# Performance work log

Hardware: AMD Instinct MI355X
Metric: run time of the kernel (lower is better)

## Reference

```python
import jax, jax.numpy as jnp
import numpy as np

B, S, HID = 2, 2048, 1024
H, D = 16, 64
R = 128  # max_relative_position
NREL = 2 * R + 1


def _make_indices():
    i = np.arange(S)[:, None]
    j = np.arange(S)[None, :]
    return np.clip(j - i + R, 0, 2 * R).astype(np.int32)  # [S, S]


def setup_inputs() -> dict:
    key = jax.random.key(0)
    ks = jax.random.split(key, 10)
    sc = 0.02
    return {
        "hidden_states": jax.random.normal(ks[0], (B, S, HID), jnp.float32),
        "st_mask": jnp.ones((B, S), jnp.float32),
        "Wq": jax.random.normal(ks[1], (HID, HID), jnp.float32) * sc,
        "bq": jnp.zeros((HID,), jnp.float32),
        "Wk": jax.random.normal(ks[2], (HID, HID), jnp.float32) * sc,
        "bk": jnp.zeros((HID,), jnp.float32),
        "Wv": jax.random.normal(ks[3], (HID, HID), jnp.float32) * sc,
        "bv": jnp.zeros((HID,), jnp.float32),
        "rel_key_emb": jax.random.normal(ks[4], (NREL, D), jnp.float32) * sc,
        "rel_val_emb": jax.random.normal(ks[5], (NREL, D), jnp.float32) * sc,
        "indices": jnp.asarray(_make_indices()),
    }


def reference(hidden_states, st_mask, Wq, bq, Wk, bk, Wv, bv, rel_key_emb, rel_val_emb, indices):
    b, s, _ = hidden_states.shape

    def heads(x):  # [B,S,HID] -> [B,H,S,D]
        return x.reshape(b, s, H, D).transpose(0, 2, 1, 3)

    q = heads(hidden_states @ Wq.T + bq)
    k = heads(hidden_states @ Wk.T + bk)
    v = heads(hidden_states @ Wv.T + bv)

    scores = jnp.einsum("bhqd,bhkd->bhqk", q, k) / jnp.sqrt(jnp.asarray(D, q.dtype))

    # relative position key bias: gather per (query, key) pair
    rel_scores = jnp.einsum("bhqd,rd->bhqr", q, rel_key_emb)  # [B,H,S,NREL]
    idx = indices[None, None]  # [1,1,S,S]
    scores = scores + jnp.take_along_axis(rel_scores, jnp.broadcast_to(idx, scores.shape), axis=3)

    mask = (1.0 - st_mask) * -10000.0  # [B,S]
    scores = scores + mask[:, None, None, :]

    probs = jax.nn.softmax(scores, axis=-1)  # dropout is identity at eval
    context = jnp.einsum("bhqk,bhkd->bhqd", probs, v)

    # scatter-add probs back onto relative buckets for the value path
    qi = jnp.arange(s)[:, None]  # [S,1] broadcasts with indices [S,S]
    rel_probs = jnp.zeros((b, H, s, NREL), probs.dtype).at[:, :, qi, indices].add(probs)
    context = context + jnp.einsum("bhqr,rd->bhqd", rel_probs, rel_val_emb)

    return context.transpose(0, 2, 1, 3).reshape(b, s, H * D)
```

## Files before the change

kernel.cpp:

```cpp
#include <hip/hip_runtime.h>
#include <math.h>

typedef __bf16 bf16;
typedef __bf16 bf16x8 __attribute__((ext_vector_type(8)));
typedef __bf16 bf16x4 __attribute__((ext_vector_type(4)));
typedef float  f32x4  __attribute__((ext_vector_type(4)));

namespace {
constexpr int B_ = 2, S_ = 2048, HID_ = 1024, H_ = 16, D_ = 64, R_ = 128, NREL_ = 257;
constexpr float LOG2E_ = 1.44269504f;
constexpr float QSC_ = 0.125f * LOG2E_;
}

static __device__ __forceinline__ f32x4 mfma16(bf16x8 a, bf16x8 b, f32x4 c) {
  return __builtin_amdgcn_mfma_f32_16x16x32_bf16(a, b, c, 0, 0, 0);
}
static __device__ __forceinline__ void split2(float f, bf16 &hi, bf16 &lo) {
  hi = (bf16)f; lo = (bf16)(f - (float)hi);
}
static __device__ __forceinline__ void gload16(const bf16* g, bf16* l) {
  __builtin_amdgcn_global_load_lds(
      (const __attribute__((address_space(1))) void*)g,
      (__attribute__((address_space(3))) void*)l, 16, 0, 0);
}

__global__ __launch_bounds__(256) void prep_kernel(
    const float* __restrict__ st_mask, const float* __restrict__ rkE,
    const float* __restrict__ rvE, const float* __restrict__ hidden,
    const float* __restrict__ Wq, const float* __restrict__ Wk,
    const float* __restrict__ Wv,
    float* __restrict__ msk2, bf16* __restrict__ rkEb, bf16* __restrict__ rvTb,
    bf16* __restrict__ Ahg, bf16* __restrict__ Alg, bf16* __restrict__ Wbg)
{
  const int t0 = blockIdx.x * 256 + threadIdx.x;
  const int NT = gridDim.x * 256;
  for (int t = t0; t < B_ * S_; t += NT)
    msk2[t] = (1.f - st_mask[t]) * -10000.f * LOG2E_;
  for (int t = t0; t < 272 * 64; t += NT) {
    const int bk = t >> 6, d = t & 63;
    rkEb[t] = (bk < NREL_) ? (bf16)(rkE[bk * D_ + d] * 8.0f) : (bf16)0.f;
  }
  for (int t = t0; t < 64 * 288; t += NT) {
    const int d = t / 288, c = t - d * 288;
    rvTb[t] = (c < NREL_) ? (bf16)rvE[c * D_ + d] : (bf16)0.f;
  }
  for (int t = t0; t < (B_ * S_ * HID_) / 4; t += NT) {
    const float4 a = ((const float4*)hidden)[t];
    const float av[4] = {a.x, a.y, a.z, a.w};
    bf16x4 h, o;
#pragma unroll
    for (int i = 0; i < 4; ++i) {
      bf16 th, tl;
      split2(av[i], th, tl);
      h[i] = th; o[i] = tl;
    }
    *(bf16x4*)&Ahg[t * 4] = h;
    *(bf16x4*)&Alg[t * 4] = o;
  }
  for (int t = t0; t < 3 * (HID_ * HID_) / 4; t += NT) {
    const int s = t >> 18, i = t & 262143;
    const float4 wv4 = ((const float4*)(s == 0 ? Wq : s == 1 ? Wk : Wv))[i];
    bf16x4 h;
    h[0] = (bf16)wv4.x; h[1] = (bf16)wv4.y; h[2] = (bf16)wv4.z; h[3] = (bf16)wv4.w;
    *(bf16x4*)&Wbg[s * 1048576 + i * 4] = h;
  }
}

__global__ __launch_bounds__(256, 2) void qkv_mfma_kernel(
    const bf16* __restrict__ Ahg, const bf16* __restrict__ Alg,
    const bf16* __restrict__ Wbg,
    const float* __restrict__ bq, const float* __restrict__ bk,
    const float* __restrict__ bv,
    bf16* __restrict__ Qh, bf16* __restrict__ Ql,
    bf16* __restrict__ Kb, bf16* __restrict__ Vt)
{
  const int swz = ((int)blockIdx.x & 7) * 64 + ((int)blockIdx.x >> 3);
  const int m0 = (swz >> 4) * 128;
  const int n0 = (swz & 15) * 64;
  const int tid = threadIdx.x;
  const int l = tid & 63, w = tid >> 6;
  const int cl = l & 15, g = l >> 4;

  __shared__ __align__(16) bf16 AhS[2][4096];
  __shared__ __align__(16) bf16 AlS[2][4096];
  __shared__ __align__(16) bf16 WS[2][3][2048];

  const int r0 = tid >> 2;
  const int csw = (((tid & 3) ^ (r0 & 3)) << 3);
  const size_t aoff0 = (size_t)(m0 + r0) * HID_ + csw;
  const size_t aoff1 = (size_t)(m0 + 64 + r0) * HID_ + csw;
  const size_t woff  = (size_t)(n0 + r0) * HID_ + csw;
  const int wb = w * 512;

  const int rA0 = w * 16 + cl;
  const int eA0 = rA0 * 32 + 8 * (g ^ (rA0 & 3));
  const int eA1 = eA0 + 2048;
  const int eW  = cl * 32 + 8 * (g ^ (cl & 3));

  f32x4 acc[2][3][4];
#pragma unroll
  for (int hf = 0; hf < 2; ++hf)
#pragma unroll
    for (int s = 0; s < 3; ++s)
#pragma unroll
      for (int nf = 0; nf < 4; ++nf)
#pragma unroll
        for (int i = 0; i < 4; ++i) acc[hf][s][nf][i] = 0.f;

  gload16(Ahg + aoff0, &AhS[0][wb]);
  gload16(Ahg + aoff1, &AhS[0][2048 + wb]);
  gload16(Alg + aoff0, &AlS[0][wb]);
  gload16(Alg + aoff1, &AlS[0][2048 + wb]);
  gload16(Wbg + woff,           &WS[0][0][wb]);
  gload16(Wbg + 1048576 + woff, &WS[0][1][wb]);
  gload16(Wbg + 2097152 + woff, &WS[0][2][wb]);
  __syncthreads();

  int cur = 0;
  for (int kt = 0; kt < HID_ / 32; ++kt) {
    if (kt + 1 < HID_ / 32) {
      const size_t ko = (size_t)(kt + 1) * 32;
      bf16* ah = &AhS[cur ^ 1][0]; bf16* al = &AlS[cur ^ 1][0];
      gload16(Ahg + aoff0 + ko, ah + wb);
      gload16(Ahg + aoff1 + ko, ah + 2048 + wb);
      gload16(Alg + aoff0 + ko, al + wb);
      gload16(Alg + aoff1 + ko, al + 2048 + wb);
      gload16(Wbg + woff + ko,           &WS[cur ^ 1][0][wb]);
      gload16(Wbg + 1048576 + woff + ko, &WS[cur ^ 1][1][wb]);
      gload16(Wbg + 2097152 + woff + ko, &WS[cur ^ 1][2][wb]);
    }

    const bf16x8 fah0 = *(const bf16x8*)&AhS[cur][eA0];
    const bf16x8 fah1 = *(const bf16x8*)&AhS[cur][eA1];
    const bf16x8 fal0 = *(const bf16x8*)&AlS[cur][eA0];
    const bf16x8 fal1 = *(const bf16x8*)&AlS[cur][eA1];
#pragma unroll
    for (int s = 0; s < 3; ++s)
#pragma unroll
      for (int nf = 0; nf < 4; ++nf) {
        const bf16x8 fb = *(const bf16x8*)&WS[cur][s][nf * 512 + eW];
        acc[0][s][nf] = mfma16(fah0, fb, acc[0][s][nf]);
        acc[0][s][nf] = mfma16(fal0, fb, acc[0][s][nf]);
        acc[1][s][nf] = mfma16(fah1, fb, acc[1][s][nf]);
        acc[1][s][nf] = mfma16(fal1, fb, acc[1][s][nf]);
      }
    __syncthreads();
    cur ^= 1;
  }

  const float* bs_[3] = {bq, bk, bv};
#pragma unroll
  for (int s = 0; s < 3; ++s)
#pragma unroll
    for (int nf = 0; nf < 4; ++nf) {
      const int n = n0 + nf * 16 + cl;
      const float bias = bs_[s][n];
      const int hd = n >> 6, d = n & 63;
#pragma unroll
      for (int hf = 0; hf < 2; ++hf)
#pragma unroll
        for (int reg = 0; reg < 4; ++reg) {
          const int m = m0 + hf * 64 + w * 16 + g * 4 + reg;
          const int b = m >> 11, sq = m & (S_ - 1);
          const float val = acc[hf][s][nf][reg] + bias;
          if (s == 0) {
            bf16 h, o; split2(val * QSC_, h, o);
            const size_t idx = ((size_t)(b * H_ + hd) * S_ + sq) * D_ + d;
            Qh[idx] = h; Ql[idx] = o;
          } else if (s == 1) {
            Kb[((size_t)(b * H_ + hd) * S_ + sq) * D_ + d] = (bf16)val;
          } else {
            Vt[(((size_t)(b * H_ + hd) * (S_ / 64) + (sq >> 6)) * D_ + d) * 64 + (sq & 63)]
                = (bf16)val;
          }
        }
    }
}

__global__ __launch_bounds__(512, 4) void attn_kernel(
    const bf16* __restrict__ Qh, const bf16* __restrict__ Ql,
    const bf16* __restrict__ Kb, const bf16* __restrict__ Vt,
    const float* __restrict__ msk2, const bf16* __restrict__ rkEb,
    const bf16* __restrict__ rvTb, float* __restrict__ out)
{
  const int swz = ((int)blockIdx.x & 7) * 128 + ((int)blockIdx.x >> 3);
  const int qt = swz & 31, h = (swz >> 5) & 15, b = swz >> 9;
  const int q0 = qt * 64;
  const int tid = threadIdx.x;
  const int l = tid & 63, w = tid >> 6;
  const int wq = (w & 3) * 16;
  const int wh = w >> 2;
  const int cl = l & 15, g = l >> 4, kg8 = g * 8;
  const int lq = wq + cl;

  __shared__ __align__(16) bf16 k_s[2][4096];
  __shared__ __align__(16) bf16 v_s[2][4096];
  __shared__ __align__(16) bf16 T[64][288];
  __shared__ __align__(16) bf16 ph[64][72];
  __shared__ float red[2][3][64];
  __shared__ float lsum_s[64];

  const size_t bh = (size_t)(b * H_ + h) * S_;
  const bf16* Kbase = Kb + bh * D_;
  const bf16* Vbase = Vt + bh * D_;
  const float* mbase = msk2 + b * S_;

  const int tKr = tid >> 3;
  const int koff = tKr * 64 + (((tid & 7) ^ (tKr & 7)) << 3);
  const int voff = koff;
  bf16* kdst0 = &k_s[0][w * 512]; bf16* kdst1 = &k_s[1][w * 512];
  bf16* vdst0 = &v_s[0][w * 512]; bf16* vdst1 = &v_s[1][w * 512];

  gload16(Kbase + koff, kdst0);
  gload16(Vbase + voff, vdst0);

  bf16x8 qh0, qh1, ql0, ql1;
  {
    const size_t base = (bh + q0 + lq) * D_ + kg8;
    qh0 = *(const bf16x8*)(Qh + base);
    qh1 = *(const bf16x8*)(Qh + base + 32);
    ql0 = *(const bf16x8*)(Ql + base);
    ql1 = *(const bf16x8*)(Ql + base + 32);
  }

  {
    const int nt0 = wh ? 9 : 0, ntE = wh ? 17 : 9;
    for (int nt = nt0; nt < ntE; ++nt) {
      f32x4 r; r[0] = r[1] = r[2] = r[3] = 0.f;
      const bf16x8 a0 = *(const bf16x8*)(rkEb + (size_t)(nt * 16 + cl) * 64 + kg8);
      const bf16x8 a1 = *(const bf16x8*)(rkEb + (size_t)(nt * 16 + cl) * 64 + 32 + kg8);
      r = mfma16(a0, qh0, r); r = mfma16(a0, ql0, r);
      r = mfma16(a1, qh1, r); r = mfma16(a1, ql1, r);
      bf16x4 pk;
#pragma unroll
      for (int reg = 0; reg < 4; ++reg) pk[reg] = (bf16)r[reg];
      *(bf16x4*)&T[lq][nt * 16 + g * 4] = pk;
    }
  }
  __syncthreads();

  const float rs_lo = (float)T[lq][0];
  const float rs_hi = (float)T[lq][2 * R_];
  const int qg = q0 + lq;

  f32x4 ctx0, ctx1;
#pragma unroll
  for (int i = 0; i < 4; ++i) { ctx0[i] = 0.f; ctx1[i] = 0.f; }
  float lsum = 0.f, plo = 0.f, phi = 0.f;

  const int r00 = wh * 32 + cl, r10 = wh * 32 + 16 + cl;
  const int e00 = r00 * 64 + 8 * (g ^ (r00 & 7)), e01 = r00 * 64 + 8 * ((4 + g) ^ (r00 & 7));
  const int e10 = r10 * 64 + 8 * (g ^ (r10 & 7)), e11 = r10 * 64 + 8 * ((4 + g) ^ (r10 & 7));
  const int f0  = e00, f0b = e01;
  const int f1  = e10, f1b = e11;

  int cur = 0;
  for (int kt = 0; kt < S_ / 64; ++kt) {
    if (kt + 1 < S_ / 64) {
      gload16(Kbase + (size_t)(kt + 1) * 4096 + koff, cur ? kdst0 : kdst1);
      gload16(Vbase + (size_t)(kt + 1) * 4096 + voff, cur ? vdst0 : vdst1);
    }

    const bf16* kc = &k_s[cur][0];
    const bf16x8 a00 = *(const bf16x8*)&kc[e00];
    const bf16x8 a01 = *(const bf16x8*)&kc[e01];
    const bf16x8 a10 = *(const bf16x8*)&kc[e10];
    const bf16x8 a11 = *(const bf16x8*)&kc[e11];

    f32x4 s0, s1;
    s0[0]=s0[1]=s0[2]=s0[3]=0.f; s1[0]=s1[1]=s1[2]=s1[3]=0.f;
    __builtin_amdgcn_s_setprio(1);
    s0 = mfma16(a00, qh0, s0); s0 = mfma16(a00, ql0, s0);
    s0 = mfma16(a01, qh1, s0); s0 = mfma16(a01, ql1, s0);
    s1 = mfma16(a10, qh0, s1); s1 = mfma16(a10, ql0, s1);
    s1 = mfma16(a11, qh1, s1); s1 = mfma16(a11, ql1, s1);
    __builtin_amdgcn_s_setprio(0);

    const int j0 = kt * 64 + wh * 32;
    const float4 mk0 = *(const float4*)(mbase + j0 + g * 4);
    const float4 mk1 = *(const float4*)(mbase + j0 + 16 + g * 4);
    const int dlt = kt * 64 - q0;
    const int mode = (dlt <= -192) ? 0 : (dlt >= 192 ? 1 : 2);

#pragma unroll
    for (int nf = 0; nf < 2; ++nf) {
      const f32x4 sa = nf ? s1 : s0;
      const float4 mkv = nf ? mk1 : mk0;
      const float mks[4] = {mkv.x, mkv.y, mkv.z, mkv.w};
      float p[4];
      if (mode == 0) {
#pragma unroll
        for (int reg = 0; reg < 4; ++reg) p[reg] = exp2f(sa[reg] + rs_lo + mks[reg]);
        plo += (p[0] + p[1]) + (p[2] + p[3]);
      } else if (mode == 1) {
#pragma unroll
        for (int reg = 0; reg < 4; ++reg) p[reg] = exp2f(sa[reg] + rs_hi + mks[reg]);
        phi += (p[0] + p[1]) + (p[2] + p[3]);
      } else {
        const int jb = j0 + nf * 16 + g * 4;
#pragma unroll
        for (int reg = 0; reg < 4; ++reg) {
          const int bkv = jb + reg - qg + R_;
          const int bkc = bkv < 0 ? 0 : (bkv > 2 * R_ ? 2 * R_ : bkv);
          const float pv = exp2f(sa[reg] + (float)T[lq][bkc] + mks[reg]);
          p[reg] = pv;
          if (bkv <= 0)           plo += pv;
          else if (bkv >= 2 * R_) phi += pv;
          else                    T[lq][bkv] = (bf16)pv;
        }
      }
      lsum += (p[0] + p[1]) + (p[2] + p[3]);
      bf16x4 pk;
#pragma unroll
      for (int reg = 0; reg < 4; ++reg) pk[reg] = (bf16)p[reg];
      *(bf16x4*)&ph[lq][wh * 32 + nf * 16 + g * 4] = pk;
    }
    __syncthreads();

    const bf16x8 pa0 = *(const bf16x8*)&ph[lq][kg8];
    const bf16x8 pa1 = *(const bf16x8*)&ph[lq][32 + kg8];
    const bf16* vc = &v_s[cur][0];
    const bf16x8 vb00 = *(const bf16x8*)&vc[f0];
    const bf16x8 vb01 = *(const bf16x8*)&vc[f0b];
    const bf16x8 vb10 = *(const bf16x8*)&vc[f1];
    const bf16x8 vb11 = *(const bf16x8*)&vc[f1b];
    __builtin_amdgcn_s_setprio(1);
    ctx0 = mfma16(pa0, vb00, ctx0); ctx0 = mfma16(pa1, vb01, ctx0);
    ctx1 = mfma16(pa0, vb10, ctx1); ctx1 = mfma16(pa1, vb11, ctx1);
    __builtin_amdgcn_s_setprio(0);
    __syncthreads();
    cur ^= 1;
  }

  lsum += __shfl_xor(lsum, 16); lsum += __shfl_xor(lsum, 32);
  plo  += __shfl_xor(plo, 16);  plo  += __shfl_xor(plo, 32);
  phi  += __shfl_xor(phi, 16);  phi  += __shfl_xor(phi, 32);
  if (l < 16) {
    red[wh][0][wq + l] = lsum;
    red[wh][1][wq + l] = plo;
    red[wh][2][wq + l] = phi;
  }
  __syncthreads();
  if (tid < 64) {
    lsum_s[tid]    = red[0][0][tid] + red[1][0][tid];
    T[tid][0]      = (bf16)(red[0][1][tid] + red[1][1][tid]);
    T[tid][2 * R_] = (bf16)(red[0][2][tid] + red[1][2][tid]);
  }
  for (int t = tid; t < 64 * 32; t += 512) {
    const int c = t & 31;
    if (c) T[t >> 5][256 + c] = (bf16)0.f;
  }
  if (q0 < R_ || q0 > S_ - R_ - 64) {
    for (int t = tid; t < 64 * 256; t += 512) {
      const int r = t >> 8, c = t & 255;
      if (c >= 1) {
        const int j = q0 + r + c - R_;
        if (j < 0 || j >= S_) T[r][c] = (bf16)0.f;
      }
    }
  }
  __syncthreads();

#pragma unroll
  for (int ks = 0; ks < 9; ++ks) {
    const bf16x8 pa = *(const bf16x8*)&T[lq][ks * 32 + kg8];
    const bf16x8 v0 = *(const bf16x8*)(rvTb + (size_t)(wh * 32 + cl) * 288 + ks * 32 + kg8);
    const bf16x8 v1 = *(const bf16x8*)(rvTb + (size_t)(wh * 32 + 16 + cl) * 288 + ks * 32 + kg8);
    __builtin_amdgcn_s_setprio(1);
    ctx0 = mfma16(pa, v0, ctx0);
    ctx1 = mfma16(pa, v1, ctx1);
    __builtin_amdgcn_s_setprio(0);
  }

#pragma unroll
  for (int reg = 0; reg < 4; ++reg) {
    const int qrow = wq + g * 4 + reg;
    const float invl = 1.f / lsum_s[qrow];
    float* op = out + (size_t)(b * S_ + q0 + qrow) * HID_ + h * 64 + wh * 32;
    op[cl]      = ctx0[reg] * invl;
    op[16 + cl] = ctx1[reg] * invl;
  }
}

extern "C" void kernel_launch(void* const* d_in, const int* in_sizes, int n_in,
                              void* d_out, int out_size, void* d_ws, size_t ws_size,
                              hipStream_t stream)
{
  (void)in_sizes; (void)n_in; (void)out_size; (void)ws_size;
  const float* hidden  = (const float*)d_in[0];
  const float* st_mask = (const float*)d_in[1];
  const float* Wq = (const float*)d_in[2];
  const float* bq = (const float*)d_in[3];
  const float* Wk = (const float*)d_in[4];
  const float* bk = (const float*)d_in[5];
  const float* Wv = (const float*)d_in[6];
  const float* bv = (const float*)d_in[7];
  const float* rkE = (const float*)d_in[8];
  const float* rvE = (const float*)d_in[9];
  float* out = (float*)d_out;

  const size_t per = (size_t)B_ * H_ * S_ * D_;
  char* wsb = (char*)d_ws;
  float* msk2 = (float*)wsb;
  bf16*  rkEb = (bf16*)(wsb + 16384);
  bf16*  rvTb = (bf16*)(wsb + 16384 + 34816);
  char*  base1 = wsb + 16384 + 34816 + 36864;
  bf16* Qh = (bf16*)base1;
  bf16* Ql = Qh + per;
  bf16* Kb = Ql + per;
  bf16* Vt = Kb + per;
  bf16* Ahg = Vt + per;
  bf16* Alg = Ahg + per;
  bf16* Wbg = Alg + per;

  prep_kernel<<<dim3(1024), 256, 0, stream>>>(
      st_mask, rkE, rvE, hidden, Wq, Wk, Wv, msk2, rkEb, rvTb, Ahg, Alg, Wbg);
  qkv_mfma_kernel<<<dim3(512), 256, 0, stream>>>(
      Ahg, Alg, Wbg, bq, bk, bv, Qh, Ql, Kb, Vt);
  attn_kernel<<<dim3(1024), 512, 0, stream>>>(
      Qh, Ql, Kb, Vt, msk2, rkEb, rvTb, out);
}
```

Baseline: 184.1 us.

## Keep P in registers for PV MFMA, split keys across wave halves, reduce ctx at end

Each wave now feeds its own softmax probabilities straight from registers into the PV MFMA. To make that work, V is stored in a permuted column order that matches the MFMA operand layout, and each wave-half accumulates all 64 output dims over its 32 keys. This removes the LDS round-trip for P and one __syncthreads per key tile. In exchange it doubles the context accumulators per wave and adds a final cross-wave reduction through shared memory, which reuses the K/V buffer space.

Measured after the change: 179.7 us. -2.4%, faster.

```diff
diff --git a/kernel.cpp b/kernel.cpp
--- a/kernel.cpp
+++ b/kernel.cpp
@@ -170,7 +170,10 @@
           } else if (s == 1) {
             Kb[((size_t)(b * H_ + hd) * S_ + sq) * D_ + d] = (bf16)val;
           } else {
-            Vt[(((size_t)(b * H_ + hd) * (S_ / 64) + (sq >> 6)) * D_ + d) * 64 + (sq & 63)]
+            const int jo = sq & 63;
+            const int mc = (jo & 32) | (((jo >> 3) & 1) << 4) | (((jo >> 2) & 1) << 3)
+                         | (((jo >> 4) & 1) << 2) | (jo & 3);
+            Vt[(((size_t)(b * H_ + hd) * (S_ / 64) + (sq >> 6)) * D_ + d) * 64 + mc]
                 = (bf16)val;
           }
         }
@@ -193,12 +196,16 @@
   const int cl = l & 15, g = l >> 4, kg8 = g * 8;
   const int lq = wq + cl;
 
-  __shared__ __align__(16) bf16 k_s[2][4096];
-  __shared__ __align__(16) bf16 v_s[2][4096];
+  __shared__ __align__(16) unsigned char U[36864];
   __shared__ __align__(16) bf16 T[64][288];
-  __shared__ __align__(16) bf16 ph[64][72];
   __shared__ float red[2][3][64];
   __shared__ float lsum_s[64];
+
+  bf16* kb0 = (bf16*)&U[0];
+  bf16* kb1 = (bf16*)&U[8192];
+  bf16* vb0 = (bf16*)&U[16384];
+  bf16* vb1 = (bf16*)&U[24576];
+  float* ctxredf = (float*)&U[0];
 
   const size_t bh = (size_t)(b * H_ + h) * S_;
   const bf16* Kbase = Kb + bh * D_;
@@ -207,12 +214,9 @@
 
   const int tKr = tid >> 3;
   const int koff = tKr * 64 + (((tid & 7) ^ (tKr & 7)) << 3);
-  const int voff = koff;
-  bf16* kdst0 = &k_s[0][w * 512]; bf16* kdst1 = &k_s[1][w * 512];
-  bf16* vdst0 = &v_s[0][w * 512]; bf16* vdst1 = &v_s[1][w * 512];
-
-  gload16(Kbase + koff, kdst0);
-  gload16(Vbase + voff, vdst0);
+
+  gload16(Kbase + koff, kb0 + w * 512);
+  gload16(Vbase + koff, vb0 + w * 512);
 
   bf16x8 qh0, qh1, ql0, ql1;
   {
@@ -243,25 +247,31 @@
   const float rs_hi = (float)T[lq][2 * R_];
   const int qg = q0 + lq;
 
-  f32x4 ctx0, ctx1;
-#pragma unroll
-  for (int i = 0; i < 4; ++i) { ctx0[i] = 0.f; ctx1[i] = 0.f; }
+  f32x4 ctx[4];
+#pragma unroll
+  for (int nf = 0; nf < 4; ++nf) { ctx[nf][0]=0.f; ctx[nf][1]=0.f; ctx[nf][2]=0.f; ctx[nf][3]=0.f; }
   float lsum = 0.f, plo = 0.f, phi = 0.f;
 
   const int r00 = wh * 32 + cl, r10 = wh * 32 + 16 + cl;
   const int e00 = r00 * 64 + 8 * (g ^ (r00 & 7)), e01 = r00 * 64 + 8 * ((4 + g) ^ (r00 & 7));
   const int e10 = r10 * 64 + 8 * (g ^ (r10 & 7)), e11 = r10 * 64 + 8 * ((4 + g) ^ (r10 & 7));
-  const int f0  = e00, f0b = e01;
-  const int f1  = e10, f1b = e11;
+  int fv0, fv1, fv2, fv3;
+  {
+    const int rd0 = 0 * 16 + cl, rd1 = 1 * 16 + cl, rd2 = 2 * 16 + cl, rd3 = 3 * 16 + cl;
+    fv0 = rd0 * 64 + 8 * ((4 * wh + g) ^ (rd0 & 7));
+    fv1 = rd1 * 64 + 8 * ((4 * wh + g) ^ (rd1 & 7));
+    fv2 = rd2 * 64 + 8 * ((4 * wh + g) ^ (rd2 & 7));
+    fv3 = rd3 * 64 + 8 * ((4 * wh + g) ^ (rd3 & 7));
+  }
 
   int cur = 0;
   for (int kt = 0; kt < S_ / 64; ++kt) {
     if (kt + 1 < S_ / 64) {
-      gload16(Kbase + (size_t)(kt + 1) * 4096 + koff, cur ? kdst0 : kdst1);
-      gload16(Vbase + (size_t)(kt + 1) * 4096 + voff, cur ? vdst0 : vdst1);
-    }
-
-    const bf16* kc = &k_s[cur][0];
+      gload16(Kbase + (size_t)(kt + 1) * 4096 + koff, (cur ? kb0 : kb1) + w * 512);
+      gload16(Vbase + (size_t)(kt + 1) * 4096 + koff, (cur ? vb0 : vb1) + w * 512);
+    }
+
+    const bf16* kc = cur ? kb1 : kb0;
     const bf16x8 a00 = *(const bf16x8*)&kc[e00];
     const bf16x8 a01 = *(const bf16x8*)&kc[e01];
     const bf16x8 a10 = *(const bf16x8*)&kc[e10];
@@ -282,6 +292,7 @@
     const int dlt = kt * 64 - q0;
     const int mode = (dlt <= -192) ? 0 : (dlt >= 192 ? 1 : 2);
 
+    bf16x4 pk0, pk1;
 #pragma unroll
     for (int nf = 0; nf < 2; ++nf) {
       const f32x4 sa = nf ? s1 : s0;
@@ -313,20 +324,18 @@
       bf16x4 pk;
 #pragma unroll
       for (int reg = 0; reg < 4; ++reg) pk[reg] = (bf16)p[reg];
-      *(bf16x4*)&ph[lq][wh * 32 + nf * 16 + g * 4] = pk;
-    }
-    __syncthreads();
-
-    const bf16x8 pa0 = *(const bf16x8*)&ph[lq][kg8];
-    const bf16x8 pa1 = *(const bf16x8*)&ph[lq][32 + kg8];
-    const bf16* vc = &v_s[cur][0];
-    const bf16x8 vb00 = *(const bf16x8*)&vc[f0];
-    const bf16x8 vb01 = *(const bf16x8*)&vc[f0b];
-    const bf16x8 vb10 = *(const bf16x8*)&vc[f1];
-    const bf16x8 vb11 = *(const bf16x8*)&vc[f1b];
+      if (nf == 0) pk0 = pk; else pk1 = pk;
+    }
+
+    bf16x8 pa;
+    pa[0] = pk0[0]; pa[1] = pk0[1]; pa[2] = pk0[2]; pa[3] = pk0[3];
+    pa[4] = pk1[0]; pa[5] = pk1[1]; pa[6] = pk1[2]; pa[7] = pk1[3];
+    const bf16* vc = cur ? vb1 : vb0;
     __builtin_amdgcn_s_setprio(1);
-    ctx0 = mfma16(pa0, vb00, ctx0); ctx0 = mfma16(pa1, vb01, ctx0);
-    ctx1 = mfma16(pa0, vb10, ctx1); ctx1 = mfma16(pa1, vb11, ctx1);
+    ctx[0] = mfma16(pa, *(const bf16x8*)&vc[fv0], ctx[0]);
+    ctx[1] = mfma16(pa, *(const bf16x8*)&vc[fv1], ctx[1]);
+    ctx[2] = mfma16(pa, *(const bf16x8*)&vc[fv2], ctx[2]);
+    ctx[3] = mfma16(pa, *(const bf16x8*)&vc[fv3], ctx[3]);
     __builtin_amdgcn_s_setprio(0);
     __syncthreads();
     cur ^= 1;
@@ -341,6 +350,15 @@
     red[wh][2][wq + l] = phi;
   }
   __syncthreads();
+
+  {
+    const int nfs = wh ? 0 : 2;
+#pragma unroll
+    for (int k2 = 0; k2 < 2; ++k2)
+#pragma unroll
+      for (int reg = 0; reg < 4; ++reg)
+        ctxredf[((wh * 64) + wq + g * 4 + reg) * 36 + k2 * 16 + cl] = ctx[nfs + k2][reg];
+  }
   if (tid < 64) {
     lsum_s[tid]    = red[0][0][tid] + red[1][0][tid];
     T[tid][0]      = (bf16)(red[0][1][tid] + red[1][1][tid]);
@@ -361,14 +379,22 @@
   }
   __syncthreads();
 
+  const int nfa = wh ? 2 : 0;
+  f32x4 cx0 = ctx[nfa], cx1 = ctx[nfa + 1];
+#pragma unroll
+  for (int reg = 0; reg < 4; ++reg) {
+    cx0[reg] += ctxredf[(((wh ^ 1) * 64) + wq + g * 4 + reg) * 36 + cl];
+    cx1[reg] += ctxredf[(((wh ^ 1) * 64) + wq + g * 4 + reg) * 36 + 16 + cl];
+  }
+
 #pragma unroll
   for (int ks = 0; ks < 9; ++ks) {
     const bf16x8 pa = *(const bf16x8*)&T[lq][ks * 32 + kg8];
     const bf16x8 v0 = *(const bf16x8*)(rvTb + (size_t)(wh * 32 + cl) * 288 + ks * 32 + kg8);
     const bf16x8 v1 = *(const bf16x8*)(rvTb + (size_t)(wh * 32 + 16 + cl) * 288 + ks * 32 + kg8);
     __builtin_amdgcn_s_setprio(1);
-    ctx0 = mfma16(pa, v0, ctx0);
-    ctx1 = mfma16(pa, v1, ctx1);
+    cx0 = mfma16(pa, v0, cx0);
+    cx1 = mfma16(pa, v1, cx1);
     __builtin_amdgcn_s_setprio(0);
   }
 
@@ -377,8 +403,8 @@
     const int qrow = wq + g * 4 + reg;
     const float invl = 1.f / lsum_s[qrow];
     float* op = out + (size_t)(b * S_ + q0 + qrow) * HID_ + h * 64 + wh * 32;
-    op[cl]      = ctx0[reg] * invl;
-    op[16 + cl] = ctx1[reg] * invl;
+    op[cl]      = cx0[reg] * invl;
+    op[16 + cl] = cx1[reg] * invl;
   }
 }
 
```
